# Optimization experiments

Hardware: AMD Instinct MI355X
Metric: run time of the kernel (lower is better)

The kernel has to match this reference:

```python
import jax, jax.numpy as jnp
import numpy as np

CUBE_SIZE = 3
RADIUS = 0.25
NSAMPLE = 512
B, N = 128, 8192


def make_centers():
    # grid of cube_size^3 centers, centered at origin, spacing = radius
    g = np.arange(CUBE_SIZE, dtype=np.float32)
    c = np.stack(np.meshgrid(g, g, g, indexing='ij'), axis=-1).reshape(-1, 3)
    c -= (CUBE_SIZE - 1) / 2.0
    c *= RADIUS
    return jnp.asarray(c[None])  # [1, P, 3]


def setup_inputs() -> dict:
    key = jax.random.key(0)
    xyz = jax.random.normal(key, (B, N, 3), dtype=jnp.float32)
    return {"xyz": xyz, "centers": make_centers()}


def reference(xyz, centers):
    # xyz: [B, N, 3], centers: [1, P, 3]
    b_, n_, _ = xyz.shape
    p_ = centers.shape[1]
    c = jnp.broadcast_to(centers, (b_, p_, 3))

    # squared distances [B, P, N] without materializing [B,P,N,3]
    x2 = jnp.sum(xyz * xyz, axis=-1)            # [B, N]
    c2 = jnp.sum(c * c, axis=-1)                # [B, P]
    xc = jnp.einsum('bpd,bnd->bpn', c, xyz)     # [B, P, N]
    dist2 = x2[:, None, :] + c2[:, :, None] - 2.0 * xc

    # ball query: first NSAMPLE points (in index order) with dist2 < r^2;
    # remaining slots padded with the first found index (0 if none found),
    # matching the PointNet++ CUDA kernel semantics.
    mask = dist2 < (RADIUS * RADIUS)
    order = jnp.where(mask, jnp.cumsum(mask, axis=-1) - 1, NSAMPLE)  # slot per point
    first_idx = jnp.argmax(mask, axis=-1)                             # [B, P], 0 if none
    idx = jnp.broadcast_to(first_idx[..., None], (b_, p_, NSAMPLE))
    bi = jnp.arange(b_)[:, None, None]
    pi = jnp.arange(p_)[None, :, None]
    js = jnp.broadcast_to(jnp.arange(n_)[None, None, :], (b_, p_, n_))
    idx = idx.at[bi, pi, order].set(js, mode='drop')                  # [B, P, NSAMPLE]

    # gather neighbors and re-center (QueryAndGroup with use_xyz, no features)
    grouped = jnp.take_along_axis(xyz[:, None, :, :], idx[..., None], axis=2)  # [B,P,S,3]
    grouped = grouped - c[:, :, None, :]

    # permute(0,2,3,1) of [B,3,P,S] -> [B,P,S,3] then merge batch and center dims
    return grouped.reshape(b_ * p_, NSAMPLE, 3)
```

## Files before the change

### kernel.cpp

```cpp
#include <hip/hip_runtime.h>


constexpr int P   = 27;
constexpr int N   = 8192;
constexpr int S   = 512;
constexpr int B   = 128;
constexpr int BLK = 256;

__global__ __launch_bounds__(1024) void pc_compact_kernel(
    const float* __restrict__ xyz, float4* __restrict__ cand,
    int* __restrict__ ccnt) {
  int b    = blockIdx.x;
  int tid  = threadIdx.x;
  int lane = tid & 63;
  int wave = tid >> 6;
  __shared__ int s_wsum[16];

  const float4* p4 = (const float4*)(xyz + (size_t)b * (N * 3));
  float4 f[6];
#pragma unroll
  for (int k = 0; k < 6; ++k) f[k] = p4[tid * 6 + k];
  float xs[8], ys[8], zs[8];
  {
    const float* fp = (const float*)f;
#pragma unroll
    for (int k = 0; k < 8; ++k) {
      xs[k] = fp[3 * k + 0]; ys[k] = fp[3 * k + 1]; zs[k] = fp[3 * k + 2];
    }
  }

  unsigned mask = 0;
#pragma unroll
  for (int k = 0; k < 8; ++k) {
    float cx = fminf(fmaxf(roundf(xs[k] * 4.0f), -1.0f), 1.0f) * 0.25f;
    float cy = fminf(fmaxf(roundf(ys[k] * 4.0f), -1.0f), 1.0f) * 0.25f;
    float cz = fminf(fmaxf(roundf(zs[k] * 4.0f), -1.0f), 1.0f) * 0.25f;
    float dx = xs[k] - cx, dy = ys[k] - cy, dz = zs[k] - cz;
    float d2 = dx * dx + dy * dy + dz * dz;
    if (d2 < 0.0625f + 1e-4f) mask |= 1u << k;
  }

  int pcnt = __popc(mask);
  int incl = pcnt;
#pragma unroll
  for (int d = 1; d < 64; d <<= 1) {
    int v = __shfl_up(incl, d);
    if (lane >= d) incl += v;
  }
  if (lane == 63) s_wsum[wave] = incl;
  __syncthreads();
  int woff = 0, total = 0;
#pragma unroll
  for (int w = 0; w < 16; ++w) {
    int c = s_wsum[w];
    if (w < wave) woff += c;
    total += c;
  }
  int pos = woff + (incl - pcnt);

  float4* cb = cand + (size_t)b * N;
#pragma unroll
  for (int k = 0; k < 8; ++k) {
    if (mask & (1u << k)) cb[pos++] = make_float4(xs[k], ys[k], zs[k], 0.0f);
  }
  if (tid == 0) ccnt[b] = total;
}

__global__ __launch_bounds__(BLK) void pc_group2_kernel(
    const float4* __restrict__ cand, const int* __restrict__ ccnt,
    const float* __restrict__ xyz, const float* __restrict__ centers,
    float* __restrict__ out) {
  int i   = blockIdx.x;
  int xcd = i & 7;
  int j   = i >> 3;
  int b   = xcd * 16 + j / P;
  int p   = j - (j / P) * P;

  float cx = centers[p * 3 + 0];
  float cy = centers[p * 3 + 1];
  float cz = centers[p * 3 + 2];
  double cxd = (double)cx, cyd = (double)cy, czd = (double)cz;

  const float4* cb = cand + (size_t)b * N;
  int cnt = ccnt[b];
  float* o = out + ((size_t)b * P + p) * (S * 3);

  __shared__ int   s_wsum[BLK / 64];
  __shared__ float s_first[3];

  int tid  = threadIdx.x;
  int wave = tid >> 6;
  int lane = tid & 63;

  int base = 0;
  for (int start = 0; start < cnt; start += BLK) {
    int idx  = start + tid;
    bool act = idx < cnt;
    float4 pt = make_float4(0.0f, 0.0f, 0.0f, 0.0f);
    if (act) pt = cb[idx];
    double dx = (double)pt.x - cxd;
    double dy = (double)pt.y - cyd;
    double dz = (double)pt.z - czd;
    double d2 = dx * dx + dy * dy + dz * dz;
    bool inball = act && (d2 < 0.0625);

    unsigned long long m = __ballot(inball);
    if (lane == 0) s_wsum[wave] = __popcll(m);
    __syncthreads();

    int woff = 0, total = 0;
#pragma unroll
    for (int w = 0; w < BLK / 64; ++w) {
      int c = s_wsum[w];
      total += c;
      if (w < wave) woff += c;
    }
    int pre  = __popcll(m & ((1ull << lane) - 1ull));
    int slot = base + woff + pre;
    if (inball && slot < S) {
      float fx = pt.x - cx, fy = pt.y - cy, fz = pt.z - cz;
      o[slot * 3 + 0] = fx;
      o[slot * 3 + 1] = fy;
      o[slot * 3 + 2] = fz;
      if (slot == 0) { s_first[0] = fx; s_first[1] = fy; s_first[2] = fz; }
    }
    base += total;
    __syncthreads();
    if (base >= S) break;
  }

  float fx, fy, fz;
  if (base > 0) {
    fx = s_first[0]; fy = s_first[1]; fz = s_first[2];
  } else {
    const float* pts = xyz + (size_t)b * (N * 3);
    fx = pts[0] - cx; fy = pts[1] - cy; fz = pts[2] - cz;
  }
  int filled = base < S ? base : S;
  for (int slot = filled + tid; slot < S; slot += BLK) {
    o[slot * 3 + 0] = fx;
    o[slot * 3 + 1] = fy;
    o[slot * 3 + 2] = fz;
  }
}

__global__ __launch_bounds__(BLK) void pc_group_kernel(
    const float* __restrict__ xyz, const float* __restrict__ centers,
    float* __restrict__ out) {
  int i = blockIdx.x;
  int xcd = i & 7;
  int j = i >> 3;
  int b = xcd * 16 + j / P;
  int p = j - (j / P) * P;

  const float* pts = xyz + (size_t)b * (N * 3);
  float cx = centers[p * 3 + 0];
  float cy = centers[p * 3 + 1];
  float cz = centers[p * 3 + 2];
  double cxd = (double)cx, cyd = (double)cy, czd = (double)cz;
  float* o = out + ((size_t)b * P + p) * (S * 3);

  __shared__ int   s_wavesum[BLK / 64];
  __shared__ float s_first[3];
  int tid = threadIdx.x, wave = tid >> 6, lane = tid & 63;

  int base = 0;
  for (int start = 0; start < N; start += BLK) {
    int n = start + tid;
    float x = pts[n * 3 + 0], y = pts[n * 3 + 1], z = pts[n * 3 + 2];
    double dx = (double)x - cxd, dy = (double)y - cyd, dz = (double)z - czd;
    bool inball = dx * dx + dy * dy + dz * dz < 0.0625;

    unsigned long long m = __ballot(inball);
    if (lane == 0) s_wavesum[wave] = __popcll(m);
    __syncthreads();
    int woff = 0, total = 0;
#pragma unroll
    for (int w = 0; w < BLK / 64; ++w) {
      int c = s_wavesum[w];
      total += c;
      if (w < wave) woff += c;
    }
    int pre = __popcll(m & ((1ull << lane) - 1ull));
    int slot = base + woff + pre;
    if (inball && slot < S) {
      float fx = x - cx, fy = y - cy, fz = z - cz;
      o[slot * 3 + 0] = fx; o[slot * 3 + 1] = fy; o[slot * 3 + 2] = fz;
      if (slot == 0) { s_first[0] = fx; s_first[1] = fy; s_first[2] = fz; }
    }
    base += total;
    __syncthreads();
    if (base >= S) break;
  }
  float fx, fy, fz;
  if (base > 0) { fx = s_first[0]; fy = s_first[1]; fz = s_first[2]; }
  else { fx = pts[0] - cx; fy = pts[1] - cy; fz = pts[2] - cz; }
  int filled = base < S ? base : S;
  for (int slot = filled + tid; slot < S; slot += BLK) {
    o[slot * 3 + 0] = fx; o[slot * 3 + 1] = fy; o[slot * 3 + 2] = fz;
  }
}

extern "C" void kernel_launch(void* const* d_in, const int* in_sizes, int n_in,
                              void* d_out, int out_size, void* d_ws, size_t ws_size,
                              hipStream_t stream) {
  const float* xyz     = (const float*)d_in[0];
  const float* centers = (const float*)d_in[1];
  float* out           = (float*)d_out;

  const size_t cand_bytes = (size_t)B * N * sizeof(float4);
  const size_t need       = cand_bytes + B * sizeof(int);

  if (ws_size >= need) {
    float4* cand = (float4*)d_ws;
    int*    ccnt = (int*)((char*)d_ws + cand_bytes);
    pc_compact_kernel<<<B, 1024, 0, stream>>>(xyz, cand, ccnt);
    pc_group2_kernel<<<B * P, BLK, 0, stream>>>(cand, ccnt, xyz, centers, out);
  } else {
    pc_group_kernel<<<B * P, BLK, 0, stream>>>(xyz, centers, out);
  }
}
```

Before: 75.33 us.

## Split compaction into regions and share candidates in LDS across wave-per-center groups

The compaction kernel now runs 8 blocks per batch, each handling a 1024-point region with its own count, which raises parallelism. The group kernel assigns one wave per center and 4 centers per block. The block loads the concatenated candidates into shared memory once, so several centers reuse them, and each wave scans with ballot and popcount without block barriers. The padding fill is vectorised with float4 stores. The cost is a 32KB LDS footprint, an idle wave in the last group of each batch (27 centers over 28 wave slots), and a fallback path that reads global memory when candidates exceed 2048.

```diff
diff --git a/kernel.cpp b/kernel.cpp
--- a/kernel.cpp
+++ b/kernel.cpp
@@ -1,37 +1,39 @@
 #include <hip/hip_runtime.h>
 
 
-constexpr int P   = 27;
-constexpr int N   = 8192;
-constexpr int S   = 512;
-constexpr int B   = 128;
-constexpr int BLK = 256;
-
-__global__ __launch_bounds__(1024) void pc_compact_kernel(
+constexpr int P    = 27;
+constexpr int N    = 8192;
+constexpr int S    = 512;
+constexpr int B    = 128;
+constexpr int NREG = 8;
+constexpr int RPTS = N / NREG;
+constexpr int CAND_MAX = 2048;
+
+__global__ __launch_bounds__(256) void pc_compact_kernel(
     const float* __restrict__ xyz, float4* __restrict__ cand,
     int* __restrict__ ccnt) {
-  int b    = blockIdx.x;
+  int blk  = blockIdx.x;
+  int b    = blk >> 3;
+  int r    = blk & 7;
   int tid  = threadIdx.x;
   int lane = tid & 63;
   int wave = tid >> 6;
-  __shared__ int s_wsum[16];
-
-  const float4* p4 = (const float4*)(xyz + (size_t)b * (N * 3));
-  float4 f[6];
-#pragma unroll
-  for (int k = 0; k < 6; ++k) f[k] = p4[tid * 6 + k];
-  float xs[8], ys[8], zs[8];
-  {
-    const float* fp = (const float*)f;
-#pragma unroll
-    for (int k = 0; k < 8; ++k) {
-      xs[k] = fp[3 * k + 0]; ys[k] = fp[3 * k + 1]; zs[k] = fp[3 * k + 2];
-    }
+  __shared__ int s_wsum[4];
+
+  const float4* p4 = (const float4*)xyz + ((size_t)b * 6144 + r * 768);
+  float4 f[3];
+#pragma unroll
+  for (int k = 0; k < 3; ++k) f[k] = p4[tid * 3 + k];
+  const float* fp = (const float*)f;
+  float xs[4], ys[4], zs[4];
+#pragma unroll
+  for (int k = 0; k < 4; ++k) {
+    xs[k] = fp[3 * k + 0]; ys[k] = fp[3 * k + 1]; zs[k] = fp[3 * k + 2];
   }
 
   unsigned mask = 0;
 #pragma unroll
-  for (int k = 0; k < 8; ++k) {
+  for (int k = 0; k < 4; ++k) {
     float cx = fminf(fmaxf(roundf(xs[k] * 4.0f), -1.0f), 1.0f) * 0.25f;
     float cy = fminf(fmaxf(roundf(ys[k] * 4.0f), -1.0f), 1.0f) * 0.25f;
     float cz = fminf(fmaxf(roundf(zs[k] * 4.0f), -1.0f), 1.0f) * 0.25f;
@@ -51,100 +53,129 @@
   __syncthreads();
   int woff = 0, total = 0;
 #pragma unroll
-  for (int w = 0; w < 16; ++w) {
+  for (int w = 0; w < 4; ++w) {
     int c = s_wsum[w];
     if (w < wave) woff += c;
     total += c;
   }
   int pos = woff + (incl - pcnt);
 
-  float4* cb = cand + (size_t)b * N;
-#pragma unroll
-  for (int k = 0; k < 8; ++k) {
+  float4* cb = cand + (size_t)b * N + r * RPTS;
+#pragma unroll
+  for (int k = 0; k < 4; ++k) {
     if (mask & (1u << k)) cb[pos++] = make_float4(xs[k], ys[k], zs[k], 0.0f);
   }
-  if (tid == 0) ccnt[b] = total;
-}
-
-__global__ __launch_bounds__(BLK) void pc_group2_kernel(
+  if (tid == 0) ccnt[blk] = total;
+}
+
+__device__ __forceinline__ void scan_region(
+    const float4* src, int cnt, float cx, float cy, float cz,
+    double cxd, double cyd, double czd, float* __restrict__ o, int lane,
+    int& base, bool& has_first, float& f0x, float& f0y, float& f0z) {
+  for (int off = 0; off < cnt && base < S; off += 64) {
+    int idx  = off + lane;
+    bool act = idx < cnt;
+    float4 pt = act ? src[idx] : make_float4(0.f, 0.f, 0.f, 0.f);
+    double dx = (double)pt.x - cxd;
+    double dy = (double)pt.y - cyd;
+    double dz = (double)pt.z - czd;
+    bool inball = act && (dx * dx + dy * dy + dz * dz < 0.0625);
+
+    unsigned long long m = __ballot(inball);
+    int pre  = __popcll(m & ((1ull << lane) - 1ull));
+    int slot = base + pre;
+    if (inball && slot < S) {
+      float fx = pt.x - cx, fy = pt.y - cy, fz = pt.z - cz;
+      o[slot * 3 + 0] = fx;
+      o[slot * 3 + 1] = fy;
+      o[slot * 3 + 2] = fz;
+      if (slot == 0) { has_first = true; f0x = fx; f0y = fy; f0z = fz; }
+    }
+    base += __popcll(m);
+  }
+}
+
+__global__ __launch_bounds__(256) void pc_group2_kernel(
     const float4* __restrict__ cand, const int* __restrict__ ccnt,
     const float* __restrict__ xyz, const float* __restrict__ centers,
     float* __restrict__ out) {
   int i   = blockIdx.x;
   int xcd = i & 7;
   int j   = i >> 3;
-  int b   = xcd * 16 + j / P;
-  int p   = j - (j / P) * P;
+  int b   = xcd * 16 + j / 7;
+  int g   = j % 7;
+  int tid = threadIdx.x, lane = tid & 63, wave = tid >> 6;
+
+  __shared__ float4 s_cand[CAND_MAX];
+
+  int c[NREG], off[NREG], ctot = 0;
+#pragma unroll
+  for (int q = 0; q < NREG; ++q) {
+    c[q] = ccnt[b * NREG + q];
+    off[q] = ctot;
+    ctot += c[q];
+  }
+  bool cached = ctot <= CAND_MAX;
+  if (cached) {
+#pragma unroll
+    for (int q = 0; q < NREG; ++q) {
+      const float4* src = cand + (size_t)b * N + q * RPTS;
+      for (int idx = tid; idx < c[q]; idx += 256) s_cand[off[q] + idx] = src[idx];
+    }
+  }
+  __syncthreads();
+
+  int p = g * 4 + wave;
+  if (p >= P) return;
 
   float cx = centers[p * 3 + 0];
   float cy = centers[p * 3 + 1];
   float cz = centers[p * 3 + 2];
   double cxd = (double)cx, cyd = (double)cy, czd = (double)cz;
-
-  const float4* cb = cand + (size_t)b * N;
-  int cnt = ccnt[b];
   float* o = out + ((size_t)b * P + p) * (S * 3);
 
-  __shared__ int   s_wsum[BLK / 64];
-  __shared__ float s_first[3];
-
-  int tid  = threadIdx.x;
-  int wave = tid >> 6;
-  int lane = tid & 63;
-
   int base = 0;
-  for (int start = 0; start < cnt; start += BLK) {
-    int idx  = start + tid;
-    bool act = idx < cnt;
-    float4 pt = make_float4(0.0f, 0.0f, 0.0f, 0.0f);
-    if (act) pt = cb[idx];
-    double dx = (double)pt.x - cxd;
-    double dy = (double)pt.y - cyd;
-    double dz = (double)pt.z - czd;
-    double d2 = dx * dx + dy * dy + dz * dz;
-    bool inball = act && (d2 < 0.0625);
-
-    unsigned long long m = __ballot(inball);
-    if (lane == 0) s_wsum[wave] = __popcll(m);
-    __syncthreads();
-
-    int woff = 0, total = 0;
-#pragma unroll
-    for (int w = 0; w < BLK / 64; ++w) {
-      int c = s_wsum[w];
-      total += c;
-      if (w < wave) woff += c;
-    }
-    int pre  = __popcll(m & ((1ull << lane) - 1ull));
-    int slot = base + woff + pre;
-    if (inball && slot < S) {
-      float fx = pt.x - cx, fy = pt.y - cy, fz = pt.z - cz;
-      o[slot * 3 + 0] = fx;
-      o[slot * 3 + 1] = fy;
-      o[slot * 3 + 2] = fz;
-      if (slot == 0) { s_first[0] = fx; s_first[1] = fy; s_first[2] = fz; }
-    }
-    base += total;
-    __syncthreads();
-    if (base >= S) break;
-  }
-
-  float fx, fy, fz;
-  if (base > 0) {
-    fx = s_first[0]; fy = s_first[1]; fz = s_first[2];
+  bool has_first = false;
+  float f0x = 0.f, f0y = 0.f, f0z = 0.f;
+  if (cached) {
+    scan_region(s_cand, ctot, cx, cy, cz, cxd, cyd, czd, o, lane,
+                base, has_first, f0x, f0y, f0z);
+  } else {
+#pragma unroll
+    for (int q = 0; q < NREG; ++q)
+      scan_region(cand + (size_t)b * N + q * RPTS, c[q], cx, cy, cz,
+                  cxd, cyd, czd, o, lane, base, has_first, f0x, f0y, f0z);
+  }
+
+  float px, py, pz;
+  unsigned long long fm = __ballot(has_first);
+  if (fm) {
+    int src = __ffsll((unsigned long long)fm) - 1;
+    px = __shfl(f0x, src); py = __shfl(f0y, src); pz = __shfl(f0z, src);
   } else {
     const float* pts = xyz + (size_t)b * (N * 3);
-    fx = pts[0] - cx; fy = pts[1] - cy; fz = pts[2] - cz;
-  }
+    px = pts[0] - cx; py = pts[1] - cy; pz = pts[2] - cz;
+  }
+
   int filled = base < S ? base : S;
-  for (int slot = filled + tid; slot < S; slot += BLK) {
-    o[slot * 3 + 0] = fx;
-    o[slot * 3 + 1] = fy;
-    o[slot * 3 + 2] = fz;
-  }
-}
-
-__global__ __launch_bounds__(BLK) void pc_group_kernel(
+  int d0 = filled * 3;
+  int hb = (d0 + 3) & ~3;
+  if (hb > 1536) hb = 1536;
+  if (lane < hb - d0) {
+    int d = d0 + lane;
+    int rr = d % 3;
+    o[d] = rr == 0 ? px : (rr == 1 ? py : pz);
+  }
+  for (int gq = (hb >> 2) + lane; gq < 1536 / 4; gq += 64) {
+    int rr = gq % 3;
+    float a = rr == 0 ? px : (rr == 1 ? py : pz);
+    float b2 = rr == 0 ? py : (rr == 1 ? pz : px);
+    float c2 = rr == 0 ? pz : (rr == 1 ? px : py);
+    ((float4*)o)[gq] = make_float4(a, b2, c2, a);
+  }
+}
+
+__global__ __launch_bounds__(256) void pc_group_kernel(
     const float* __restrict__ xyz, const float* __restrict__ centers,
     float* __restrict__ out) {
   int i = blockIdx.x;
@@ -160,12 +191,12 @@
   double cxd = (double)cx, cyd = (double)cy, czd = (double)cz;
   float* o = out + ((size_t)b * P + p) * (S * 3);
 
-  __shared__ int   s_wavesum[BLK / 64];
+  __shared__ int   s_wavesum[4];
   __shared__ float s_first[3];
   int tid = threadIdx.x, wave = tid >> 6, lane = tid & 63;
 
   int base = 0;
-  for (int start = 0; start < N; start += BLK) {
+  for (int start = 0; start < N; start += 256) {
     int n = start + tid;
     float x = pts[n * 3 + 0], y = pts[n * 3 + 1], z = pts[n * 3 + 2];
     double dx = (double)x - cxd, dy = (double)y - cyd, dz = (double)z - czd;
@@ -176,10 +207,10 @@
     __syncthreads();
     int woff = 0, total = 0;
 #pragma unroll
-    for (int w = 0; w < BLK / 64; ++w) {
-      int c = s_wavesum[w];
-      total += c;
-      if (w < wave) woff += c;
+    for (int w = 0; w < 4; ++w) {
+      int cc = s_wavesum[w];
+      total += cc;
+      if (w < wave) woff += cc;
     }
     int pre = __popcll(m & ((1ull << lane) - 1ull));
     int slot = base + woff + pre;
@@ -196,7 +227,7 @@
   if (base > 0) { fx = s_first[0]; fy = s_first[1]; fz = s_first[2]; }
   else { fx = pts[0] - cx; fy = pts[1] - cy; fz = pts[2] - cz; }
   int filled = base < S ? base : S;
-  for (int slot = filled + tid; slot < S; slot += BLK) {
+  for (int slot = filled + tid; slot < S; slot += 256) {
     o[slot * 3 + 0] = fx; o[slot * 3 + 1] = fy; o[slot * 3 + 2] = fz;
   }
 }
@@ -209,14 +240,14 @@
   float* out           = (float*)d_out;
 
   const size_t cand_bytes = (size_t)B * N * sizeof(float4);
-  const size_t need       = cand_bytes + B * sizeof(int);
+  const size_t need       = cand_bytes + (size_t)B * NREG * sizeof(int);
 
   if (ws_size >= need) {
     float4* cand = (float4*)d_ws;
     int*    ccnt = (int*)((char*)d_ws + cand_bytes);
-    pc_compact_kernel<<<B, 1024, 0, stream>>>(xyz, cand, ccnt);
-    pc_group2_kernel<<<B * P, BLK, 0, stream>>>(cand, ccnt, xyz, centers, out);
+    pc_compact_kernel<<<B * NREG, 256, 0, stream>>>(xyz, cand, ccnt);
+    pc_group2_kernel<<<B * 7, 256, 0, stream>>>(cand, ccnt, xyz, centers, out);
   } else {
-    pc_group_kernel<<<B * P, BLK, 0, stream>>>(xyz, centers, out);
-  }
-}
+    pc_group_kernel<<<B * P, 256, 0, stream>>>(xyz, centers, out);
+  }
+}
```

After: 76.72 us. No clear change (+1.8%).
